# Performance work log

Hardware: AMD Instinct MI355X
Metric: run time of the kernel (lower is better)

## Reference

```python
import jax, jax.numpy as jnp
import numpy as np

T, N, E, B, H = 16, 20000, 320000, 16, 64
NEG_SLOPE = 0.2


def gat_conv(x, src, dst, W, att_s, att_d, bias):
    # x: [N, Fin]; W: [Fin, heads*C]; att_s/att_d: [heads, C]; bias: [heads*C]
    n = x.shape[0]
    heads, C = att_s.shape
    h = (x @ W).reshape(n, heads, C)                      # [N, heads, C]
    a_s = (h * att_s).sum(-1)                             # [N, heads]
    a_d = (h * att_d).sum(-1)                             # [N, heads]
    e = jax.nn.leaky_relu(a_s[src] + a_d[dst], NEG_SLOPE)  # [E, heads]
    e_max = jax.ops.segment_max(e, dst, num_segments=n)
    e = jnp.exp(e - e_max[dst])
    denom = jax.ops.segment_sum(e, dst, num_segments=n)
    alpha = e / (denom[dst] + 1e-16)                      # softmax over in-edges
    msg = h[src] * alpha[:, :, None]                      # [E, heads, C]
    out = jax.ops.segment_sum(msg, dst, num_segments=n)   # [N, heads, C]
    return out.reshape(n, heads * C) + bias


def encode_frame(x, ei, batch, params):
    W1, as1, ad1, b1, W2, as2, ad2, b2 = params
    loop = jnp.arange(N)
    src = jnp.concatenate([ei[0], loop])  # add self-loops (PyG default)
    dst = jnp.concatenate([ei[1], loop])
    h = jax.nn.elu(gat_conv(x, src, dst, W1, as1, ad1, b1))   # [N, 64]
    h = jax.nn.elu(gat_conv(h, src, dst, W2, as2, ad2, b2))   # [N, 64]
    sums = jax.ops.segment_sum(h, batch, num_segments=B)       # [B, 64]
    cnt = jax.ops.segment_sum(jnp.ones((N,), h.dtype), batch, num_segments=B)
    return sums / jnp.maximum(cnt, 1.0)[:, None]


def gru(x_seq, Wih, Whh, bih, bhh):
    # x_seq: [T, B, H]; torch gate order r, z, n
    def step(h, x_t):
        gx = x_t @ Wih.T + bih
        gh = h @ Whh.T + bhh
        xr, xz, xn = jnp.split(gx, 3, axis=-1)
        hr, hz, hn = jnp.split(gh, 3, axis=-1)
        r = jax.nn.sigmoid(xr + hr)
        z = jax.nn.sigmoid(xz + hz)
        n = jnp.tanh(xn + r * hn)
        h_new = (1.0 - z) * n + z * h
        return h_new, None
    h0 = jnp.zeros((x_seq.shape[1], H), x_seq.dtype)
    h_n, _ = jax.lax.scan(step, h0, x_seq)
    return h_n


def setup_inputs() -> dict:
    key = jax.random.key(0)
    ks = jax.random.split(key, 20)
    s = 0.1
    return {
        "x": jax.random.normal(ks[0], (T, N, 7), jnp.float32),
        "edge_index": jax.random.randint(ks[1], (T, 2, E), 0, N),
        "batch": jnp.sort(jax.random.randint(ks[2], (T, N), 0, B), axis=-1),
        "W1": jax.random.normal(ks[3], (7, 2 * 32), jnp.float32) * s,
        "att_src1": jax.random.normal(ks[4], (2, 32), jnp.float32) * s,
        "att_dst1": jax.random.normal(ks[5], (2, 32), jnp.float32) * s,
        "b1": jnp.zeros((64,), jnp.float32),
        "W2": jax.random.normal(ks[6], (64, 64), jnp.float32) * s,
        "att_src2": jax.random.normal(ks[7], (1, 64), jnp.float32) * s,
        "att_dst2": jax.random.normal(ks[8], (1, 64), jnp.float32) * s,
        "b2": jnp.zeros((64,), jnp.float32),
        "Wih": jax.random.normal(ks[9], (3 * H, H), jnp.float32) * s,
        "Whh": jax.random.normal(ks[10], (3 * H, H), jnp.float32) * s,
        "bih": jnp.zeros((3 * H,), jnp.float32),
        "bhh": jnp.zeros((3 * H,), jnp.float32),
        "Wc1": jax.random.normal(ks[11], (H, 32), jnp.float32) * s,
        "bc1": jnp.zeros((32,), jnp.float32),
        "Wc2": jax.random.normal(ks[12], (32, 1), jnp.float32) * s,
        "bc2": jnp.zeros((1,), jnp.float32),
    }


def reference(x, edge_index, batch, W1, att_src1, att_dst1, b1, W2, att_src2,
              att_dst2, b2, Wih, Whh, bih, bhh, Wc1, bc1, Wc2, bc2):
    gat_params = (W1, att_src1, att_dst1, b1, W2, att_src2, att_dst2, b2)
    emb = jax.vmap(lambda xf, ef, bf: encode_frame(xf, ef, bf, gat_params))(
        x, edge_index, batch)                 # [T, B, 64]
    h_n = gru(emb, Wih, Whh, bih, bhh)        # [B, 64]
    hid = jax.nn.relu(h_n @ Wc1 + bc1)        # dropout is eval-mode identity
    logits = hid @ Wc2 + bc2                  # [B, 1]
    return logits
```

## Files before the change

### kernel.cpp

```cpp
#include <hip/hip_runtime.h>
#include <math.h>

#define T_ 16
#define N_ 20000
#define E_ 320000
#define EN_ (E_ + N_)
#define B_ 16
#define RPF 32
#define RNODES (N_ / RPF)
#define SLICE_CAP 12544
#define BCAP 13000
#define CPB 64
#define CHUNK4 (E_ / 4 / CPB)

__device__ __forceinline__ float lrelu(float v) { return v >= 0.f ? v : 0.2f * v; }
__device__ __forceinline__ float elu(float v) { return v > 0.f ? v : expm1f(v); }
__device__ __forceinline__ float rdlane(float v, int k) {
    return __uint_as_float(__builtin_amdgcn_readlane(__float_as_uint(v), k));
}

__device__ __forceinline__ void frame_map(int bid, int* frame, int* local) {
    int blk = bid >> 3;
    *frame = (bid & 7) * 2 + (blk & 1);
    *local = blk >> 1;
}

__global__ __launch_bounds__(256) void k_h1(
    const float* __restrict__ x, const float* __restrict__ W1,
    const float* __restrict__ as1, const float* __restrict__ ad1,
    float* __restrict__ h1, float* __restrict__ a_s, float* __restrict__ a_d) {
    int lane = threadIdx.x & 63;
    int wid = (blockIdx.x * blockDim.x + threadIdx.x) >> 6;
    int nw = (gridDim.x * blockDim.x) >> 6;
    float w[7];
#pragma unroll
    for (int k = 0; k < 7; ++k) w[k] = W1[k * 64 + lane];
    float asl = as1[lane], adl = ad1[lane];
    float xv = (wid < T_ * N_ && lane < 7) ? x[(size_t)wid * 7 + lane] : 0.f;
    for (int r = wid; r < T_ * N_; r += nw) {
        float xcur = xv;
        int rn = r + nw;
        if (rn < T_ * N_ && lane < 7) xv = x[(size_t)rn * 7 + lane];
        float acc = 0.f;
#pragma unroll
        for (int k = 0; k < 7; ++k) acc = fmaf(rdlane(xcur, k), w[k], acc);
        h1[(size_t)r * 64 + lane] = acc;
        float s = acc * asl, d = acc * adl;
#pragma unroll
        for (int m = 1; m < 32; m <<= 1) { s += __shfl_xor(s, m); d += __shfl_xor(d, m); }
        if ((lane & 31) == 0) {
            a_s[r * 2 + (lane >> 5)] = s;
            a_d[r * 2 + (lane >> 5)] = d;
        }
    }
}

__global__ __launch_bounds__(256) void k_bfill2(const int* __restrict__ ei,
                                                int* __restrict__ gcur,
                                                int* __restrict__ bucket) {
    int t = blockIdx.x & 15, c = blockIdx.x >> 4;
    __shared__ int cl[RPF];
    __shared__ int rbase[RPF];
    if (threadIdx.x < RPF) cl[threadIdx.x] = 0;
    __syncthreads();
    const int4* db4 = (const int4*)(ei + (size_t)t * 2 * E_ + E_) + c * CHUNK4;
    const int4* sb4 = (const int4*)(ei + (size_t)t * 2 * E_) + c * CHUNK4;
    for (int i = threadIdx.x; i < CHUNK4; i += 256) {
        int4 d = db4[i];
        atomicAdd(&cl[d.x / RNODES], 1);
        atomicAdd(&cl[d.y / RNODES], 1);
        atomicAdd(&cl[d.z / RNODES], 1);
        atomicAdd(&cl[d.w / RNODES], 1);
    }
    __syncthreads();
    if (threadIdx.x < RPF) {
        rbase[threadIdx.x] = atomicAdd(&gcur[t * RPF + threadIdx.x], cl[threadIdx.x]);
        cl[threadIdx.x] = 0;
    }
    __syncthreads();
    for (int i = threadIdx.x; i < CHUNK4; i += 256) {
        int4 d = db4[i];
        int4 s = sb4[i];
        int b, dl, p;
        b = d.x / RNODES; dl = d.x - b * RNODES;
        p = rbase[b] + atomicAdd(&cl[b], 1);
        bucket[(size_t)(t * RPF + b) * BCAP + p] = (dl << 15) | s.x;
        b = d.y / RNODES; dl = d.y - b * RNODES;
        p = rbase[b] + atomicAdd(&cl[b], 1);
        bucket[(size_t)(t * RPF + b) * BCAP + p] = (dl << 15) | s.y;
        b = d.z / RNODES; dl = d.z - b * RNODES;
        p = rbase[b] + atomicAdd(&cl[b], 1);
        bucket[(size_t)(t * RPF + b) * BCAP + p] = (dl << 15) | s.z;
        b = d.w / RNODES; dl = d.w - b * RNODES;
        p = rbase[b] + atomicAdd(&cl[b], 1);
        bucket[(size_t)(t * RPF + b) * BCAP + p] = (dl << 15) | s.w;
    }
}

__global__ __launch_bounds__(256) void k_scat2(const int* __restrict__ bucket,
                                               const int* __restrict__ gcur,
                                               int* __restrict__ rowptr,
                                               int* __restrict__ col) {
    int t = blockIdx.x & 15, rg = blockIdx.x >> 4;
    __shared__ int hist[RNODES];
    __shared__ int cur[RNODES];
    __shared__ int colL[SLICE_CAP];
    __shared__ int wsum[4];
    __shared__ int carryS;
    int tid = threadIdx.x, lane = tid & 63, wv = tid >> 6;
    int vcnt = (lane < RPF) ? gcur[t * RPF + lane] : 0;
    int sc = vcnt;
#pragma unroll
    for (int off = 1; off < RPF; off <<= 1) {
        int u = __shfl_up(sc, off);
        if (lane >= off) sc += u;
    }
    int cnt = __shfl(vcnt, rg);
    int inclAt = __shfl(sc, rg);
    int sliceBase = (inclAt - cnt) + rg * RNODES;
    int r0 = rg * RNODES;
    const int* bk = bucket + (size_t)(t * RPF + rg) * BCAP;
    bool ovf = (cnt + RNODES) > SLICE_CAP;
    int* rp = rowptr + t * (N_ + 1);
    int* cf = col + (size_t)t * EN_;
    for (int i = tid; i < RNODES; i += 256) hist[i] = 0;
    if (tid == 0) carryS = 0;
    __syncthreads();
    for (int i = tid; i < cnt; i += 256) atomicAdd(&hist[bk[i] >> 15], 1);
    __syncthreads();
    for (int base = 0; base < RNODES; base += 256) {
        int i = base + tid;
        int v = (i < RNODES) ? hist[i] + 1 : 0;
        int s = v;
#pragma unroll
        for (int off = 1; off < 64; off <<= 1) {
            int u = __shfl_up(s, off);
            if (lane >= off) s += u;
        }
        if (lane == 63) wsum[wv] = s;
        __syncthreads();
        if (tid == 0) {
            int a = 0;
#pragma unroll
            for (int w2 = 0; w2 < 4; ++w2) { int x2 = wsum[w2]; wsum[w2] = a; a += x2; }
        }
        __syncthreads();
        int incl = s + wsum[wv] + carryS;
        if (i < RNODES) {
            cur[i] = incl - v;
            rp[r0 + i + 1] = sliceBase + incl;
        }
        __syncthreads();
        if (tid == 255) carryS = incl;
        __syncthreads();
    }
    if (rg == 0 && tid == 0) rp[0] = 0;
    __syncthreads();
    for (int i = tid; i < cnt; i += 256) {
        int e = bk[i];
        int dl = e >> 15, src = e & 0x7FFF;
        int p = atomicAdd(&cur[dl], 1);
        if (ovf) cf[sliceBase + p] = src; else colL[p] = src;
    }
    __syncthreads();
    for (int i = tid; i < RNODES; i += 256) {
        int p = cur[i];
        if (ovf) cf[sliceBase + p] = r0 + i; else colL[p] = r0 + i;
    }
    __syncthreads();
    if (!ovf) {
        int len = cnt + RNODES;
        for (int i = tid; i < len; i += 256) cf[sliceBase + i] = colL[i];
    }
}

template <int HEADS>
__global__ __launch_bounds__(256) void k_agg(
    const int* __restrict__ rowptr, const int* __restrict__ col,
    const float* __restrict__ a_s, const float* __restrict__ a_d,
    const float* __restrict__ hin, const float* __restrict__ bias,
    float* __restrict__ outp) {
    int t, local;
    frame_map(blockIdx.x, &t, &local);
    int lane = threadIdx.x & 63;
    int n = local * 4 + (threadIdx.x >> 6);
    if (n >= N_) return;
    int node = t * N_ + n;
    float ad0 = a_d[node * HEADS];
    float ad1 = (HEADS == 2) ? a_d[node * HEADS + 1] : 0.f;
    int e0 = __builtin_amdgcn_readfirstlane(rowptr[t * (N_ + 1) + n]);
    int e1 = __builtin_amdgcn_readfirstlane(rowptr[t * (N_ + 1) + n + 1]);
    const int* cb = col + (size_t)t * EN_;
    const float* hb = hin + (size_t)t * N_ * 64;
    const float* ab = a_s + (size_t)t * N_ * HEADS;
    float acc0 = 0.f, acc1 = 0.f, acc2 = 0.f, acc3 = 0.f, den0 = 0.f, den1 = 0.f;
    for (int base = e0; base < e1; base += 64) {
        int rem = e1 - base; if (rem > 64) rem = 64;
        int s = 0; float p0 = 0.f, p1 = 0.f;
        if (lane < rem) {
            s = cb[base + lane];
            if (HEADS == 2) {
                float2 av = *(const float2*)(ab + s * 2);
                p0 = expf(lrelu(av.x + ad0));
                p1 = expf(lrelu(av.y + ad1));
            } else {
                p0 = expf(lrelu(ab[s] + ad0));
            }
        }
        den0 += p0; den1 += p1;
        int k = 0;
        for (; k + 4 <= rem; k += 4) {
            int sa = __builtin_amdgcn_readlane(s, k);
            int sb = __builtin_amdgcn_readlane(s, k + 1);
            int sc = __builtin_amdgcn_readlane(s, k + 2);
            int sd = __builtin_amdgcn_readlane(s, k + 3);
            float pa, pb, pc, pd;
            if (HEADS == 2) {
                pa = (lane < 32) ? rdlane(p0, k) : rdlane(p1, k);
                pb = (lane < 32) ? rdlane(p0, k + 1) : rdlane(p1, k + 1);
                pc = (lane < 32) ? rdlane(p0, k + 2) : rdlane(p1, k + 2);
                pd = (lane < 32) ? rdlane(p0, k + 3) : rdlane(p1, k + 3);
            } else {
                pa = rdlane(p0, k); pb = rdlane(p0, k + 1);
                pc = rdlane(p0, k + 2); pd = rdlane(p0, k + 3);
            }
            acc0 = fmaf(pa, hb[((size_t)sa << 6) + lane], acc0);
            acc1 = fmaf(pb, hb[((size_t)sb << 6) + lane], acc1);
            acc2 = fmaf(pc, hb[((size_t)sc << 6) + lane], acc2);
            acc3 = fmaf(pd, hb[((size_t)sd << 6) + lane], acc3);
        }
        for (; k < rem; ++k) {
            int sa = __builtin_amdgcn_readlane(s, k);
            float pa = (HEADS == 2) ? ((lane < 32) ? rdlane(p0, k) : rdlane(p1, k))
                                    : rdlane(p0, k);
            acc0 = fmaf(pa, hb[((size_t)sa << 6) + lane], acc0);
        }
    }
    float acc = (acc0 + acc1) + (acc2 + acc3);
#pragma unroll
    for (int m = 1; m < 64; m <<= 1) {
        den0 += __shfl_xor(den0, m);
        if (HEADS == 2) den1 += __shfl_xor(den1, m);
    }
    float den = (HEADS == 2) ? ((lane < 32) ? den0 : den1) : den0;
    outp[(size_t)node * 64 + lane] = elu(acc / (den + 1e-16f) + bias[lane]);
}

__global__ __launch_bounds__(256) void k_h2(
    const float* __restrict__ xin, const float* __restrict__ W2,
    const float* __restrict__ as2, const float* __restrict__ ad2,
    float* __restrict__ h2, float* __restrict__ a_s, float* __restrict__ a_d) {
    int lane = threadIdx.x & 63;
    int wid = (blockIdx.x * blockDim.x + threadIdx.x) >> 6;
    int nw = (gridDim.x * blockDim.x) >> 6;
    float w[64];
#pragma unroll
    for (int k = 0; k < 64; ++k) w[k] = W2[k * 64 + lane];
    float asl = as2[lane], adl = ad2[lane];
    float xv = (wid < T_ * N_) ? xin[(size_t)wid * 64 + lane] : 0.f;
    for (int r = wid; r < T_ * N_; r += nw) {
        float xcur = xv;
        int rn = r + nw;
        if (rn < T_ * N_) xv = xin[(size_t)rn * 64 + lane];
        float acc = 0.f;
#pragma unroll
        for (int k = 0; k < 64; ++k) acc = fmaf(rdlane(xcur, k), w[k], acc);
        h2[(size_t)r * 64 + lane] = acc;
        float s = acc * asl, d = acc * adl;
#pragma unroll
        for (int m = 1; m < 64; m <<= 1) { s += __shfl_xor(s, m); d += __shfl_xor(d, m); }
        if (lane == 0) { a_s[r] = s; a_d[r] = d; }
    }
}

__global__ void k_pool(const float* __restrict__ hact, const int* __restrict__ batch,
                       float* __restrict__ sums, float* __restrict__ cnt) {
    int wid = (blockIdx.x * blockDim.x + threadIdx.x) >> 6;
    int lane = threadIdx.x & 63;
    const int WPF = (N_ + 63) / 64;
    int t = wid / WPF, w = wid - t * WPF;
    if (t >= T_) return;
    int n0 = w * 64, n1 = min(n0 + 64, N_);
    float acc = 0.f, cacc = 0.f;
    int cur_b = batch[t * N_ + n0];
    for (int n = n0; n < n1; ++n) {
        int b = batch[t * N_ + n];
        if (b != cur_b) {
            atomicAdd(&sums[(t * B_ + cur_b) * 64 + lane], acc);
            if (lane == 0) atomicAdd(&cnt[t * B_ + cur_b], cacc);
            acc = 0.f; cacc = 0.f; cur_b = b;
        }
        acc += hact[(size_t)(t * N_ + n) * 64 + lane];
        cacc += 1.f;
    }
    atomicAdd(&sums[(t * B_ + cur_b) * 64 + lane], acc);
    if (lane == 0) atomicAdd(&cnt[t * B_ + cur_b], cacc);
}

__global__ void k_emb(const float* __restrict__ sums, const float* __restrict__ cnt,
                      float* __restrict__ emb) {
    int idx = blockIdx.x * blockDim.x + threadIdx.x;
    if (idx >= T_ * B_ * 64) return;
    emb[idx] = sums[idx] / fmaxf(cnt[idx >> 6], 1.0f);
}

__global__ void k_gx(const float* __restrict__ emb, const float* __restrict__ Wih,
                     const float* __restrict__ bih, float* __restrict__ gx) {
    int idx = blockIdx.x * blockDim.x + threadIdx.x;
    if (idx >= T_ * B_ * 192) return;
    int tb = idx / 192, g = idx - tb * 192;
    const float* er = emb + tb * 64;
    const float* wr = Wih + g * 64;
    float acc = bih[g];
#pragma unroll
    for (int k = 0; k < 64; ++k) acc = fmaf(er[k], wr[k], acc);
    gx[idx] = acc;
}

__global__ __launch_bounds__(1024) void k_gru(
    const float* __restrict__ gx_all, const float* __restrict__ Whh,
    const float* __restrict__ bhh, const float* __restrict__ Wc1,
    const float* __restrict__ bc1, const float* __restrict__ Wc2,
    const float* __restrict__ bc2, float* __restrict__ out) {
    __shared__ float Wh[192 * 65];
    __shared__ float hL[16 * 64];
    __shared__ float gh[16 * 192];
    __shared__ float hid[16 * 32];
    int tid = threadIdx.x;
    for (int i = tid; i < 192 * 64; i += 1024) Wh[(i >> 6) * 65 + (i & 63)] = Whh[i];
    hL[tid] = 0.f;
    __syncthreads();
    for (int t = 0; t < T_; ++t) {
        for (int idx = tid; idx < 16 * 192; idx += 1024) {
            int b = idx / 192, g = idx - b * 192;
            float acc = bhh[g];
            const float* wr = Wh + g * 65;
            const float* hr = hL + b * 64;
#pragma unroll
            for (int k = 0; k < 64; ++k) acc = fmaf(hr[k], wr[k], acc);
            gh[idx] = acc;
        }
        __syncthreads();
        const float* gxt = gx_all + t * 16 * 192;
        {
            int b = tid >> 6, c = tid & 63;
            float xr = gxt[b * 192 + c], xz = gxt[b * 192 + 64 + c], xn = gxt[b * 192 + 128 + c];
            float hr_ = gh[b * 192 + c], hz = gh[b * 192 + 64 + c], hn = gh[b * 192 + 128 + c];
            float r = 1.f / (1.f + expf(-(xr + hr_)));
            float z = 1.f / (1.f + expf(-(xz + hz)));
            float n = tanhf(xn + r * hn);
            hL[tid] = (1.f - z) * n + z * hL[tid];
        }
        __syncthreads();
    }
    for (int idx = tid; idx < 16 * 32; idx += 1024) {
        int b = idx >> 5, j = idx & 31;
        float acc = bc1[j];
#pragma unroll
        for (int k = 0; k < 64; ++k) acc = fmaf(hL[b * 64 + k], Wc1[k * 32 + j], acc);
        hid[idx] = fmaxf(acc, 0.f);
    }
    __syncthreads();
    if (tid < 16) {
        float acc = bc2[0];
#pragma unroll
        for (int k = 0; k < 32; ++k) acc = fmaf(hid[tid * 32 + k], Wc2[k], acc);
        out[tid] = acc;
    }
}

extern "C" void kernel_launch(void* const* d_in, const int* in_sizes, int n_in,
                              void* d_out, int out_size, void* d_ws, size_t ws_size,
                              hipStream_t stream) {
    const float* x   = (const float*)d_in[0];
    const int*   ei  = (const int*)d_in[1];
    const int* batch = (const int*)d_in[2];
    const float* W1  = (const float*)d_in[3];
    const float* as1 = (const float*)d_in[4];
    const float* ad1 = (const float*)d_in[5];
    const float* b1  = (const float*)d_in[6];
    const float* W2  = (const float*)d_in[7];
    const float* as2 = (const float*)d_in[8];
    const float* ad2 = (const float*)d_in[9];
    const float* b2  = (const float*)d_in[10];
    const float* Wih = (const float*)d_in[11];
    const float* Whh = (const float*)d_in[12];
    const float* bih = (const float*)d_in[13];
    const float* bhh = (const float*)d_in[14];
    const float* Wc1 = (const float*)d_in[15];
    const float* bc1 = (const float*)d_in[16];
    const float* Wc2 = (const float*)d_in[17];
    const float* bc2 = (const float*)d_in[18];
    float* out = (float*)d_out;

    float* ws = (float*)d_ws;
    float* hA     = ws;
    float* hX     = hA + 20480000;
    float* a_s    = hX + 20480000;
    float* a_d    = a_s + 640000;
    int*   rowptr = (int*)(a_d + 640000);
    int*   col    = rowptr + 320032;
    float* sums   = (float*)(col + 5440000);
    float* cnt    = sums + 16384;
    float* emb    = cnt + 256;
    float* gx     = emb + 16384;
    int*   gcur   = (int*)(gx + 49152);
    int*   bucket = (int*)hA;

    const int BPF_AGG = (N_ + 3) / 4;

    hipMemsetAsync(gcur, 0, (size_t)512 * 4, stream);
    hipMemsetAsync(sums, 0, (size_t)(16384 + 256) * 4, stream);

    k_bfill2<<<16 * CPB, 256, 0, stream>>>(ei, gcur, bucket);
    k_scat2<<<16 * RPF, 256, 0, stream>>>(bucket, gcur, rowptr, col);

    k_h1<<<1024, 256, 0, stream>>>(x, W1, as1, ad1, hA, a_s, a_d);
    k_agg<2><<<16 * BPF_AGG, 256, 0, stream>>>(rowptr, col, a_s, a_d, hA, b1, hX);

    k_h2<<<1024, 256, 0, stream>>>(hX, W2, as2, ad2, hA, a_s, a_d);
    k_agg<1><<<16 * BPF_AGG, 256, 0, stream>>>(rowptr, col, a_s, a_d, hA, b2, hX);

    {
        const int WPF = (N_ + 63) / 64;
        int waves = T_ * WPF;
        k_pool<<<(waves * 64 + 255) / 256, 256, 0, stream>>>(hX, batch, sums, cnt);
    }
    k_emb<<<(T_ * B_ * 64 + 255) / 256, 256, 0, stream>>>(sums, cnt, emb);
    k_gx<<<(T_ * B_ * 192 + 255) / 256, 256, 0, stream>>>(emb, Wih, bih, gx);
    k_gru<<<1, 1024, 0, stream>>>(gx, Whh, bhh, Wc1, bc1, Wc2, bc2, out);
}
```

Baseline: 871.5 us.

## Fold GAT linear projections into aggregation using associativity of attention sums

Precomputes W·att vectors so attention logits come straight from the raw inputs. Layer 1 aggregates the 7-dim raw features per head and applies W1 afterwards, and layer 2 aggregates 64-dim inputs and applies W2 after the sum. This removes the separate h1/h2 projection kernels and their full-size intermediate writes and reads. In exchange, layer 1 does per-lane scalar gathers of 7 floats with 14-wide reductions, layer 2 runs a persistent-style loop with W2 held in registers, and the reordered floating-point sums change rounding slightly.

```diff
diff --git a/kernel.cpp b/kernel.cpp
--- a/kernel.cpp
+++ b/kernel.cpp
@@ -12,6 +12,7 @@
 #define BCAP 13000
 #define CPB 64
 #define CHUNK4 (E_ / 4 / CPB)
+#define BLK2 1250
 
 __device__ __forceinline__ float lrelu(float v) { return v >= 0.f ? v : 0.2f * v; }
 __device__ __forceinline__ float elu(float v) { return v > 0.f ? v : expm1f(v); }
@@ -25,33 +26,31 @@
     *local = blk >> 1;
 }
 
-__global__ __launch_bounds__(256) void k_h1(
-    const float* __restrict__ x, const float* __restrict__ W1,
-    const float* __restrict__ as1, const float* __restrict__ ad1,
-    float* __restrict__ h1, float* __restrict__ a_s, float* __restrict__ a_d) {
-    int lane = threadIdx.x & 63;
-    int wid = (blockIdx.x * blockDim.x + threadIdx.x) >> 6;
-    int nw = (gridDim.x * blockDim.x) >> 6;
-    float w[7];
-#pragma unroll
-    for (int k = 0; k < 7; ++k) w[k] = W1[k * 64 + lane];
-    float asl = as1[lane], adl = ad1[lane];
-    float xv = (wid < T_ * N_ && lane < 7) ? x[(size_t)wid * 7 + lane] : 0.f;
-    for (int r = wid; r < T_ * N_; r += nw) {
-        float xcur = xv;
-        int rn = r + nw;
-        if (rn < T_ * N_ && lane < 7) xv = x[(size_t)rn * 7 + lane];
-        float acc = 0.f;
-#pragma unroll
-        for (int k = 0; k < 7; ++k) acc = fmaf(rdlane(xcur, k), w[k], acc);
-        h1[(size_t)r * 64 + lane] = acc;
-        float s = acc * asl, d = acc * adl;
-#pragma unroll
-        for (int m = 1; m < 32; m <<= 1) { s += __shfl_xor(s, m); d += __shfl_xor(d, m); }
-        if ((lane & 31) == 0) {
-            a_s[r * 2 + (lane >> 5)] = s;
-            a_d[r * 2 + (lane >> 5)] = d;
-        }
+__global__ void k_proj(const float* __restrict__ W1, const float* __restrict__ as1,
+                       const float* __restrict__ ad1, const float* __restrict__ W2,
+                       const float* __restrict__ as2, const float* __restrict__ ad2,
+                       float* __restrict__ proj) {
+    int tid = threadIdx.x;
+    if (tid < 14) {
+        int h = tid / 7, c = tid - h * 7;
+        float s = 0.f;
+        for (int j = 0; j < 32; ++j) s += W1[c * 64 + h * 32 + j] * as1[h * 32 + j];
+        proj[tid] = s;
+    } else if (tid < 28) {
+        int u = tid - 14, h = u / 7, c = u - h * 7;
+        float s = 0.f;
+        for (int j = 0; j < 32; ++j) s += W1[c * 64 + h * 32 + j] * ad1[h * 32 + j];
+        proj[14 + u] = s;
+    } else if (tid >= 32 && tid < 96) {
+        int k = tid - 32;
+        float s = 0.f;
+        for (int j = 0; j < 64; ++j) s += W2[k * 64 + j] * as2[j];
+        proj[32 + k] = s;
+    } else if (tid >= 96 && tid < 160) {
+        int k = tid - 96;
+        float s = 0.f;
+        for (int j = 0; j < 64; ++j) s += W2[k * 64 + j] * ad2[j];
+        proj[96 + k] = s;
     }
 }
 
@@ -174,102 +173,144 @@
     }
 }
 
-template <int HEADS>
-__global__ __launch_bounds__(256) void k_agg(
+__global__ __launch_bounds__(256) void k_agg1(
     const int* __restrict__ rowptr, const int* __restrict__ col,
-    const float* __restrict__ a_s, const float* __restrict__ a_d,
-    const float* __restrict__ hin, const float* __restrict__ bias,
-    float* __restrict__ outp) {
+    const float* __restrict__ x, const float* __restrict__ proj,
+    const float* __restrict__ W1, const float* __restrict__ b1,
+    float* __restrict__ out1, float* __restrict__ a_s2, float* __restrict__ a_d2) {
     int t, local;
     frame_map(blockIdx.x, &t, &local);
     int lane = threadIdx.x & 63;
     int n = local * 4 + (threadIdx.x >> 6);
     if (n >= N_) return;
     int node = t * N_ + n;
-    float ad0 = a_d[node * HEADS];
-    float ad1 = (HEADS == 2) ? a_d[node * HEADS + 1] : 0.f;
+    const float* xb = x + (size_t)t * N_ * 7;
+    float vs[14], vd[14];
+#pragma unroll
+    for (int i = 0; i < 14; ++i) vs[i] = proj[i];
+#pragma unroll
+    for (int i = 0; i < 14; ++i) vd[i] = proj[14 + i];
+    float ad0 = 0.f, ad1 = 0.f;
+#pragma unroll
+    for (int c = 0; c < 7; ++c) {
+        float xc = xb[n * 7 + c];
+        ad0 = fmaf(xc, vd[c], ad0);
+        ad1 = fmaf(xc, vd[7 + c], ad1);
+    }
     int e0 = __builtin_amdgcn_readfirstlane(rowptr[t * (N_ + 1) + n]);
     int e1 = __builtin_amdgcn_readfirstlane(rowptr[t * (N_ + 1) + n + 1]);
     const int* cb = col + (size_t)t * EN_;
-    const float* hb = hin + (size_t)t * N_ * 64;
-    const float* ab = a_s + (size_t)t * N_ * HEADS;
-    float acc0 = 0.f, acc1 = 0.f, acc2 = 0.f, acc3 = 0.f, den0 = 0.f, den1 = 0.f;
+    float xa0[7] = {0.f, 0.f, 0.f, 0.f, 0.f, 0.f, 0.f};
+    float xa1[7] = {0.f, 0.f, 0.f, 0.f, 0.f, 0.f, 0.f};
+    float den0 = 0.f, den1 = 0.f;
     for (int base = e0; base < e1; base += 64) {
         int rem = e1 - base; if (rem > 64) rem = 64;
-        int s = 0; float p0 = 0.f, p1 = 0.f;
         if (lane < rem) {
-            s = cb[base + lane];
-            if (HEADS == 2) {
-                float2 av = *(const float2*)(ab + s * 2);
-                p0 = expf(lrelu(av.x + ad0));
-                p1 = expf(lrelu(av.y + ad1));
-            } else {
-                p0 = expf(lrelu(ab[s] + ad0));
+            int s = cb[base + lane];
+            float xr[7];
+#pragma unroll
+            for (int c = 0; c < 7; ++c) xr[c] = xb[s * 7 + c];
+            float as0 = 0.f, as1v = 0.f;
+#pragma unroll
+            for (int c = 0; c < 7; ++c) {
+                as0 = fmaf(xr[c], vs[c], as0);
+                as1v = fmaf(xr[c], vs[7 + c], as1v);
             }
-        }
-        den0 += p0; den1 += p1;
-        int k = 0;
-        for (; k + 4 <= rem; k += 4) {
-            int sa = __builtin_amdgcn_readlane(s, k);
-            int sb = __builtin_amdgcn_readlane(s, k + 1);
-            int sc = __builtin_amdgcn_readlane(s, k + 2);
-            int sd = __builtin_amdgcn_readlane(s, k + 3);
-            float pa, pb, pc, pd;
-            if (HEADS == 2) {
-                pa = (lane < 32) ? rdlane(p0, k) : rdlane(p1, k);
-                pb = (lane < 32) ? rdlane(p0, k + 1) : rdlane(p1, k + 1);
-                pc = (lane < 32) ? rdlane(p0, k + 2) : rdlane(p1, k + 2);
-                pd = (lane < 32) ? rdlane(p0, k + 3) : rdlane(p1, k + 3);
-            } else {
-                pa = rdlane(p0, k); pb = rdlane(p0, k + 1);
-                pc = rdlane(p0, k + 2); pd = rdlane(p0, k + 3);
+            float p0 = expf(lrelu(as0 + ad0));
+            float p1 = expf(lrelu(as1v + ad1));
+            den0 += p0; den1 += p1;
+#pragma unroll
+            for (int c = 0; c < 7; ++c) {
+                xa0[c] = fmaf(p0, xr[c], xa0[c]);
+                xa1[c] = fmaf(p1, xr[c], xa1[c]);
             }
-            acc0 = fmaf(pa, hb[((size_t)sa << 6) + lane], acc0);
-            acc1 = fmaf(pb, hb[((size_t)sb << 6) + lane], acc1);
-            acc2 = fmaf(pc, hb[((size_t)sc << 6) + lane], acc2);
-            acc3 = fmaf(pd, hb[((size_t)sd << 6) + lane], acc3);
-        }
-        for (; k < rem; ++k) {
-            int sa = __builtin_amdgcn_readlane(s, k);
-            float pa = (HEADS == 2) ? ((lane < 32) ? rdlane(p0, k) : rdlane(p1, k))
-                                    : rdlane(p0, k);
-            acc0 = fmaf(pa, hb[((size_t)sa << 6) + lane], acc0);
-        }
-    }
-    float acc = (acc0 + acc1) + (acc2 + acc3);
+        }
+    }
 #pragma unroll
     for (int m = 1; m < 64; m <<= 1) {
         den0 += __shfl_xor(den0, m);
-        if (HEADS == 2) den1 += __shfl_xor(den1, m);
-    }
-    float den = (HEADS == 2) ? ((lane < 32) ? den0 : den1) : den0;
-    outp[(size_t)node * 64 + lane] = elu(acc / (den + 1e-16f) + bias[lane]);
-}
-
-__global__ __launch_bounds__(256) void k_h2(
+        den1 += __shfl_xor(den1, m);
+#pragma unroll
+        for (int c = 0; c < 7; ++c) {
+            xa0[c] += __shfl_xor(xa0[c], m);
+            xa1[c] += __shfl_xor(xa1[c], m);
+        }
+    }
+    int head = lane >> 5;
+    float den = head ? den1 : den0;
+    float m_ = 0.f;
+#pragma unroll
+    for (int c = 0; c < 7; ++c) {
+        float xc = head ? xa1[c] : xa0[c];
+        m_ = fmaf(xc, W1[c * 64 + lane], m_);
+    }
+    float o = elu(m_ / (den + 1e-16f) + b1[lane]);
+    out1[(size_t)node * 64 + lane] = o;
+    float s2 = o * proj[32 + lane], d2 = o * proj[96 + lane];
+#pragma unroll
+    for (int m = 1; m < 64; m <<= 1) { s2 += __shfl_xor(s2, m); d2 += __shfl_xor(d2, m); }
+    if (lane == 0) { a_s2[node] = s2; a_d2[node] = d2; }
+}
+
+__global__ __launch_bounds__(256) void k_agg2(
+    const int* __restrict__ rowptr, const int* __restrict__ col,
+    const float* __restrict__ a_s, const float* __restrict__ a_d,
     const float* __restrict__ xin, const float* __restrict__ W2,
-    const float* __restrict__ as2, const float* __restrict__ ad2,
-    float* __restrict__ h2, float* __restrict__ a_s, float* __restrict__ a_d) {
+    const float* __restrict__ b2, float* __restrict__ out2) {
+    int bid = blockIdx.x;
+    int xcd = bid & 7, blk = bid >> 3;
+    int t = xcd * 2 + (blk >= BLK2 ? 1 : 0);
+    int local = (blk >= BLK2) ? blk - BLK2 : blk;
     int lane = threadIdx.x & 63;
-    int wid = (blockIdx.x * blockDim.x + threadIdx.x) >> 6;
-    int nw = (gridDim.x * blockDim.x) >> 6;
-    float w[64];
-#pragma unroll
-    for (int k = 0; k < 64; ++k) w[k] = W2[k * 64 + lane];
-    float asl = as2[lane], adl = ad2[lane];
-    float xv = (wid < T_ * N_) ? xin[(size_t)wid * 64 + lane] : 0.f;
-    for (int r = wid; r < T_ * N_; r += nw) {
-        float xcur = xv;
-        int rn = r + nw;
-        if (rn < T_ * N_) xv = xin[(size_t)rn * 64 + lane];
-        float acc = 0.f;
-#pragma unroll
-        for (int k = 0; k < 64; ++k) acc = fmaf(rdlane(xcur, k), w[k], acc);
-        h2[(size_t)r * 64 + lane] = acc;
-        float s = acc * asl, d = acc * adl;
-#pragma unroll
-        for (int m = 1; m < 64; m <<= 1) { s += __shfl_xor(s, m); d += __shfl_xor(d, m); }
-        if (lane == 0) { a_s[r] = s; a_d[r] = d; }
+    float w2[64];
+#pragma unroll
+    for (int k = 0; k < 64; ++k) w2[k] = W2[k * 64 + lane];
+    float bl = b2[lane];
+    const int* cb = col + (size_t)t * EN_;
+    const float* hb = xin + (size_t)t * N_ * 64;
+    const float* ab = a_s + (size_t)t * N_;
+    const float* adb = a_d + (size_t)t * N_;
+    const int* rp = rowptr + t * (N_ + 1);
+    float* ob = out2 + (size_t)t * N_ * 64;
+    for (int n = local * 4 + (threadIdx.x >> 6); n < N_; n += BLK2 * 4) {
+        float adv = adb[n];
+        int e0 = __builtin_amdgcn_readfirstlane(rp[n]);
+        int e1 = __builtin_amdgcn_readfirstlane(rp[n + 1]);
+        float acc0 = 0.f, acc1 = 0.f, acc2 = 0.f, acc3 = 0.f, den = 0.f;
+        for (int base = e0; base < e1; base += 64) {
+            int rem = e1 - base; if (rem > 64) rem = 64;
+            int s = 0; float p = 0.f;
+            if (lane < rem) {
+                s = cb[base + lane];
+                p = expf(lrelu(ab[s] + adv));
+                den += p;
+            }
+            int k = 0;
+            for (; k + 4 <= rem; k += 4) {
+                int sa = __builtin_amdgcn_readlane(s, k);
+                int sb = __builtin_amdgcn_readlane(s, k + 1);
+                int scx = __builtin_amdgcn_readlane(s, k + 2);
+                int sd = __builtin_amdgcn_readlane(s, k + 3);
+                float pa = rdlane(p, k), pb = rdlane(p, k + 1);
+                float pc = rdlane(p, k + 2), pd = rdlane(p, k + 3);
+                acc0 = fmaf(pa, hb[((size_t)sa << 6) + lane], acc0);
+                acc1 = fmaf(pb, hb[((size_t)sb << 6) + lane], acc1);
+                acc2 = fmaf(pc, hb[((size_t)scx << 6) + lane], acc2);
+                acc3 = fmaf(pd, hb[((size_t)sd << 6) + lane], acc3);
+            }
+            for (; k < rem; ++k) {
+                int sa = __builtin_amdgcn_readlane(s, k);
+                float pa = rdlane(p, k);
+                acc0 = fmaf(pa, hb[((size_t)sa << 6) + lane], acc0);
+            }
+        }
+        float msg = (acc0 + acc1) + (acc2 + acc3);
+#pragma unroll
+        for (int m = 1; m < 64; m <<= 1) den += __shfl_xor(den, m);
+        float hm = 0.f;
+#pragma unroll
+        for (int k = 0; k < 64; ++k) hm = fmaf(rdlane(msg, k), w2[k], hm);
+        ob[(size_t)n * 64 + lane] = elu(hm / (den + 1e-16f) + bl);
     }
 }
 
@@ -394,17 +435,18 @@
     float* out = (float*)d_out;
 
     float* ws = (float*)d_ws;
-    float* hA     = ws;
-    float* hX     = hA + 20480000;
-    float* a_s    = hX + 20480000;
-    float* a_d    = a_s + 640000;
-    int*   rowptr = (int*)(a_d + 640000);
+    float* hX     = ws;
+    float* hA     = hX + 20480000;
+    float* a_s2   = hA + 20480000;
+    float* a_d2   = a_s2 + 320000;
+    int*   rowptr = (int*)(a_d2 + 320000);
     int*   col    = rowptr + 320032;
     float* sums   = (float*)(col + 5440000);
     float* cnt    = sums + 16384;
     float* emb    = cnt + 256;
     float* gx     = emb + 16384;
     int*   gcur   = (int*)(gx + 49152);
+    float* proj   = (float*)(gcur + 512);
     int*   bucket = (int*)hA;
 
     const int BPF_AGG = (N_ + 3) / 4;
@@ -415,16 +457,16 @@
     k_bfill2<<<16 * CPB, 256, 0, stream>>>(ei, gcur, bucket);
     k_scat2<<<16 * RPF, 256, 0, stream>>>(bucket, gcur, rowptr, col);
 
-    k_h1<<<1024, 256, 0, stream>>>(x, W1, as1, ad1, hA, a_s, a_d);
-    k_agg<2><<<16 * BPF_AGG, 256, 0, stream>>>(rowptr, col, a_s, a_d, hA, b1, hX);
-
-    k_h2<<<1024, 256, 0, stream>>>(hX, W2, as2, ad2, hA, a_s, a_d);
-    k_agg<1><<<16 * BPF_AGG, 256, 0, stream>>>(rowptr, col, a_s, a_d, hA, b2, hX);
+    k_proj<<<1, 256, 0, stream>>>(W1, as1, ad1, W2, as2, ad2, proj);
+
+    k_agg1<<<16 * BPF_AGG, 256, 0, stream>>>(rowptr, col, x, proj, W1, b1, hX, a_s2, a_d2);
+
+    k_agg2<<<16 * BLK2, 256, 0, stream>>>(rowptr, col, a_s2, a_d2, hX, W2, b2, hA);
 
     {
         const int WPF = (N_ + 63) / 64;
         int waves = T_ * WPF;
-        k_pool<<<(waves * 64 + 255) / 256, 256, 0, stream>>>(hX, batch, sums, cnt);
+        k_pool<<<(waves * 64 + 255) / 256, 256, 0, stream>>>(hA, batch, sums, cnt);
     }
     k_emb<<<(T_ * B_ * 64 + 255) / 256, 256, 0, stream>>>(sums, cnt, emb);
     k_gx<<<(T_ * B_ * 192 + 255) / 256, 256, 0, stream>>>(emb, Wih, bih, gx);
```

Result: slower. 957.4 us (+9.9%).
